# Optimization experiments

Hardware: AMD Instinct MI355X
Metric: run time of the kernel (lower is better)

The kernel has to match this reference:

```python
import jax, jax.numpy as jnp
import numpy as np
from jax import lax

R_NOBOUNDARY, R_BOUNDARY, SMALL_M, BIG_M = 5, 20, 3, 6
NUM_CLASSES, EMBED = 20, 2048


def _conv1d(x, w, pad):
    # x: [B, Cin, T], w: [Cout, Cin, K] -> [B, Cout, T]
    return lax.conv_general_dilated(x, w, (1,), [(pad, pad)],
                                    dimension_numbers=('NCH', 'OIH', 'NCH'))


def _erode(b, k):
    # scipy binary_erosion with structure ones((1,k)), border_value=0:
    # out[i] = min over window [i - k//2, i + k-1 - k//2], zero-padded
    c = k // 2
    xp = jnp.pad(b, ((0, 0), (c, k - 1 - c)))
    return lax.reduce_window(xp, jnp.inf, lax.min, (1, k), (1, 1), 'VALID')


def _dilate(b, k):
    # scipy binary_dilation reflects the structure: window [i-(k-1-c), i+c]
    c = k // 2
    xp = jnp.pad(b, ((0, 0), (k - 1 - c, c)))
    return lax.reduce_window(xp, -jnp.inf, lax.max, (1, k), (1, 1), 'VALID')


def _select_topk(scores, emb, k):
    # scores: [B,T], emb: [B,T,D] -> ([B,k,D], [B,k])
    _, idx = lax.top_k(scores, k)
    sel = jnp.take_along_axis(emb, idx[:, :, None], axis=1)
    return sel, idx


def setup_inputs() -> dict:
    key = jax.random.key(0)
    ks = jax.random.split(key, 6)
    B, T = 16, 750
    x = jax.random.normal(ks[0], (B, T, 2048), dtype=jnp.float32)
    s_embed = 1.0 / np.sqrt(1024 * 3)
    w_rgb = jax.random.normal(ks[1], (EMBED, 1024, 3), dtype=jnp.float32) * s_embed
    b_rgb = jnp.zeros((EMBED,), dtype=jnp.float32)
    w_flow = jax.random.normal(ks[2], (EMBED, 1024, 3), dtype=jnp.float32) * s_embed
    b_flow = jnp.zeros((EMBED,), dtype=jnp.float32)
    w_cls = jax.random.normal(ks[3], (NUM_CLASSES, EMBED, 1), dtype=jnp.float32) / np.sqrt(EMBED)
    return {'x': x, 'w_rgb': w_rgb, 'b_rgb': b_rgb, 'w_flow': w_flow,
            'b_flow': b_flow, 'w_cls': w_cls}


def reference(x, w_rgb, b_rgb, w_flow, b_flow, w_cls):
    # Dropout layers are identity (eval mode).
    T = x.shape[1]
    k_nb = T // R_NOBOUNDARY
    k_b = T // R_BOUNDARY

    rgb = jnp.transpose(x[:, :, 0:1024], (0, 2, 1))    # [B,1024,T]
    flow = jnp.transpose(x[:, :, 1024:2048], (0, 2, 1))
    out = (jax.nn.relu(_conv1d(rgb, w_rgb, 1) + b_rgb[None, :, None])
           + jax.nn.relu(_conv1d(flow, w_flow, 1) + b_flow[None, :, None]))  # [B,2048,T]
    embeddings = jnp.transpose(out, (0, 2, 1))          # [B,T,2048]
    cas = jnp.transpose(jax.nn.relu(_conv1d(out, w_cls, 0)), (0, 2, 1))  # [B,T,C]
    actionness = cas.sum(axis=2)                        # [B,T]

    # no-boundary mining (dropout identity in eval)
    act_rev = jnp.max(actionness, axis=1, keepdims=True) - actionness
    EA, idx = _select_topk(actionness, embeddings, k_nb)
    EB, _ = _select_topk(act_rev, embeddings, k_nb)

    # boundary mining via 1D morphology on binarized actionness
    med = jnp.median(actionness, axis=1, keepdims=True)
    aness_bin = (actionness > med).astype(actionness.dtype)  # [B,T]
    inner = _erode(aness_bin, SMALL_M) - _erode(aness_bin, BIG_M)
    HA, _ = _select_topk(actionness * inner, embeddings, k_b)
    outer = _dilate(aness_bin, BIG_M) - _dilate(aness_bin, SMALL_M)
    HB, _ = _select_topk(actionness * outer, embeddings, k_b)

    # video-level class scores: per-class top-k mean over time, softmax over classes
    cas_ct = jnp.transpose(cas, (0, 2, 1))              # [B,C,T]
    topk_scores, _ = lax.top_k(cas_ct, k_nb)            # [B,C,k_nb]
    video_scores = jax.nn.softmax(topk_scores.mean(axis=2), axis=1)  # [B,C]

    return (video_scores, EA, EB, HA, HB, idx, actionness, cas, embeddings)
```

## Files before the change

### kernel.cpp

```cpp
#include <hip/hip_runtime.h>
#include <stdint.h>
#include <math.h>

#define B_   16
#define T_   750
#define NC_  20
#define KNB_ 150
#define KB_  37

typedef _Float16 f16x8 __attribute__((ext_vector_type(8)));
typedef _Float16 f16x4 __attribute__((ext_vector_type(4)));
typedef float    f32x4 __attribute__((ext_vector_type(4)));
typedef float    f32x16 __attribute__((ext_vector_type(16)));

static constexpr long long O_VS  = 0;
static constexpr long long O_EA  = 320;
static constexpr long long O_EB  = 320 + 4915200LL;
static constexpr long long O_HA  = 320 + 2*4915200LL;
static constexpr long long O_HB  = O_HA + 1212416LL;
static constexpr long long O_IDX = O_HB + 1212416LL;
static constexpr long long O_ACT = O_IDX + 2400LL;
static constexpr long long O_CAS = O_ACT + 12000LL;
static constexpr long long O_EMB = O_CAS + 240000LL;

static constexpr long long WX_ELE   = 16LL * 752 * 2048;
static constexpr long long W_XHI    = 0;
static constexpr long long W_XLO    = W_XHI + WX_ELE * 2;
static constexpr long long WW_ELE   = 2LL * 16 * 32 * 12288;
static constexpr long long W_WHI    = W_XLO + WX_ELE * 2;
static constexpr long long W_WLO    = W_WHI + WW_ELE * 2;
static constexpr long long W_SEL    = W_WLO + WW_ELE * 2;
static constexpr long long W_VS     = W_SEL + 40960;
static constexpr long long W_NEED   = W_VS + 4096;

__device__ __forceinline__ void gload16(const void* g, void* l) {
    __builtin_amdgcn_global_load_lds(
        (const __attribute__((address_space(1))) unsigned int*)g,
        (__attribute__((address_space(3))) unsigned int*)l, 16, 0, 0);
}

__global__ __launch_bounds__(256) void xsplit(
    const float* __restrict__ x, _Float16* __restrict__ xh, _Float16* __restrict__ xl)
{
    long i = (long)blockIdx.x * 256 + threadIdx.x;
    int row = (int)(i >> 9);
    int c4  = (int)(i & 511);
    int b = row / 752, tr = row - b * 752;
    int t = tr - 1;
    float4 v = make_float4(0.f, 0.f, 0.f, 0.f);
    if (t >= 0 && t < T_)
        v = *reinterpret_cast<const float4*>(x + ((long)(b * T_ + t) * 2048 + c4 * 4));
    float vv[4] = {v.x, v.y, v.z, v.w};
    f16x4 h, l;
    #pragma unroll
    for (int j = 0; j < 4; ++j) {
        _Float16 hi = (_Float16)vv[j];
        h[j] = hi;
        l[j] = (_Float16)(vv[j] - (float)hi);
    }
    long o = (long)row * 2048 + c4 * 4;
    *reinterpret_cast<f16x4*>(xh + o) = h;
    *reinterpret_cast<f16x4*>(xl + o) = l;
}

__global__ __launch_bounds__(64) void wsplit(
    const float* __restrict__ w_rgb, const float* __restrict__ w_flow,
    _Float16* __restrict__ wh, _Float16* __restrict__ wl)
{
    const int br   = blockIdx.x >> 11;
    const int co_g = blockIdx.x & 2047;
    const int tid  = threadIdx.x;
    const float* w = (br ? w_flow : w_rgb) + (long)co_g * 3072;
    __shared__ float wsrc[3072];
    for (int i = tid; i < 768; i += 64)
        reinterpret_cast<float4*>(wsrc)[i] = reinterpret_cast<const float4*>(w)[i];
    __syncthreads();
    const int nt = co_g >> 7, co = co_g & 127;
    for (int p = tid; p < 384; p += 64) {
        int oct = p / 3, k = p - oct * 3;
        int chunk = oct >> 2, g = oct & 3;
        int q = g ^ ((co >> 1) & 3);
        f16x8 h, l;
        #pragma unroll
        for (int j = 0; j < 8; ++j) {
            float v = wsrc[(oct * 8 + j) * 3 + k] * 512.f;
            _Float16 hi = (_Float16)v;
            h[j] = hi;
            l[j] = (_Float16)(v - (float)hi);
        }
        long o = ((long)(br * 16 + nt) * 32 + chunk) * 12288 + k * 4096 + co * 32 + q * 8;
        *reinterpret_cast<f16x8*>(wh + o) = h;
        *reinterpret_cast<f16x8*>(wl + o) = l;
    }
}

template<int ADD>
__global__ __launch_bounds__(256, 2) void conv_mfma(
    const _Float16* __restrict__ xh, const _Float16* __restrict__ xl,
    const _Float16* __restrict__ wh, const _Float16* __restrict__ wl,
    const float* __restrict__ bias, float* __restrict__ emb)
{
    __shared__ _Float16 XhL[6272], XlL[6272];
    __shared__ _Float16 WhL[12288], WlL[12288];

    const int tid  = threadIdx.x;
    const int lane = tid & 63;
    const int wid  = tid >> 6;
    const int wm = wid >> 1, wn = wid & 1;
    const int l31 = lane & 31, lg2 = lane >> 5;

    const int bid = blockIdx.y * 16 + blockIdx.x;
    const int lid = (bid & 7) * 128 + (bid >> 3);
    const int nt  = lid >> 6;
    const int bty = lid & 63;
    const int b   = bty >> 2;
    const int tt  = bty & 3;
    const int t0  = tt * 192;

    f32x16 acc[3][2];
    #pragma unroll
    for (int m = 0; m < 3; ++m)
        #pragma unroll
        for (int n = 0; n < 2; ++n)
            #pragma unroll
            for (int e = 0; e < 16; ++e) acc[m][n][e] = 0.f;

    const long xrowbase = (long)b * 752 + t0;
    for (int chunk = 0; chunk < 32; ++chunk) {
        const int cibase = ADD * 1024 + chunk * 32;
        for (int s = tid; s < 776; s += 256) {
            int r = s >> 2, q = s & 3;
            int g = q ^ ((r >> 1) & 3);
            long goff = (xrowbase + r) * 2048 + cibase + g * 8;
            int lbase = (s & ~63) * 8;
            gload16(xh + goff, XhL + lbase);
            gload16(xl + goff, XlL + lbase);
        }
        const long wbase = ((long)(ADD * 16 + nt) * 32 + chunk) * 12288;
        for (int s = tid; s < 1536; s += 256) {
            int lbase = (s & ~63) * 8;
            gload16(wh + wbase + (long)s * 8, WhL + lbase);
            gload16(wl + wbase + (long)s * 8, WlL + lbase);
        }
        __syncthreads();

        #pragma unroll
        for (int k = 0; k < 3; ++k) {
            #pragma unroll
            for (int s2 = 0; s2 < 2; ++s2) {
                const int g = 2 * s2 + lg2;
                f16x8 ah[3], al[3], bh[2], bl[2];
                #pragma unroll
                for (int m = 0; m < 3; ++m) {
                    int r = wm * 96 + m * 32 + l31 + k;
                    int off = r * 32 + ((g ^ ((r >> 1) & 3)) * 8);
                    ah[m] = *reinterpret_cast<const f16x8*>(&XhL[off]);
                    al[m] = *reinterpret_cast<const f16x8*>(&XlL[off]);
                }
                #pragma unroll
                for (int n = 0; n < 2; ++n) {
                    int co = wn * 64 + n * 32 + l31;
                    int off = k * 4096 + co * 32 + ((g ^ ((co >> 1) & 3)) * 8);
                    bh[n] = *reinterpret_cast<const f16x8*>(&WhL[off]);
                    bl[n] = *reinterpret_cast<const f16x8*>(&WlL[off]);
                }
                #pragma unroll
                for (int m = 0; m < 3; ++m)
                    #pragma unroll
                    for (int n = 0; n < 2; ++n) {
                        acc[m][n] = __builtin_amdgcn_mfma_f32_32x32x16_f16(ah[m], bh[n], acc[m][n], 0, 0, 0);
                        acc[m][n] = __builtin_amdgcn_mfma_f32_32x32x16_f16(al[m], bh[n], acc[m][n], 0, 0, 0);
                        acc[m][n] = __builtin_amdgcn_mfma_f32_32x32x16_f16(ah[m], bl[n], acc[m][n], 0, 0, 0);
                    }
            }
        }
        __syncthreads();
    }

    const float sc = 1.f / 512.f;
    #pragma unroll
    for (int n = 0; n < 2; ++n) {
        const int co = nt * 128 + wn * 64 + n * 32 + l31;
        const float bs = bias[co];
        #pragma unroll
        for (int m = 0; m < 3; ++m) {
            #pragma unroll
            for (int reg = 0; reg < 16; ++reg) {
                int row32 = (reg & 3) + 8 * (reg >> 2) + 4 * lg2;
                int t = t0 + wm * 96 + m * 32 + row32;
                if (t < T_) {
                    long o = ((long)b * T_ + t) * 2048 + co;
                    float v = fmaxf(fmaf(acc[m][n][reg], sc, bs), 0.f);
                    if (ADD) emb[o] += v;
                    else     emb[o]  = v;
                }
            }
        }
    }
}

__global__ __launch_bounds__(320) void cas_tc(
    const float* __restrict__ emb, const float* __restrict__ wcls,
    float* __restrict__ cas, float* __restrict__ act)
{
    const int t0g = blockIdx.x * 16;
    const int tid = threadIdx.x;
    const int tl  = tid / 20, c = tid % 20;
    __shared__ float embS[16][132];
    __shared__ float wS[20][132];
    __shared__ float casS[16][20];

    float acc = 0.f;
    for (int cc = 0; cc < 2048; cc += 128) {
        for (int s = tid; s < 512; s += 320) {
            int r = s >> 5, q = s & 31;
            *reinterpret_cast<float4*>(&embS[r][q * 4]) =
                *reinterpret_cast<const float4*>(&emb[((long)t0g + r) * 2048 + cc + q * 4]);
        }
        for (int s = tid; s < 640; s += 320) {
            int r = s >> 5, q = s & 31;
            *reinterpret_cast<float4*>(&wS[r][q * 4]) =
                *reinterpret_cast<const float4*>(&wcls[(long)r * 2048 + cc + q * 4]);
        }
        __syncthreads();
        #pragma unroll
        for (int q = 0; q < 32; ++q) {
            float4 a = *reinterpret_cast<const float4*>(&embS[tl][q * 4]);
            float4 w = *reinterpret_cast<const float4*>(&wS[c][q * 4]);
            acc = fmaf(a.x, w.x, acc); acc = fmaf(a.y, w.y, acc);
            acc = fmaf(a.z, w.z, acc); acc = fmaf(a.w, w.w, acc);
        }
        __syncthreads();
    }
    float r = acc > 0.f ? acc : 0.f;
    cas[(long)(t0g + tl) * NC_ + c] = r;
    casS[tl][c] = r;
    __syncthreads();
    if (tid < 16) {
        float s = 0.f;
        #pragma unroll
        for (int c2 = 0; c2 < NC_; ++c2) s += casS[tid][c2];
        act[t0g + tid] = s;
    }
}

__global__ __launch_bounds__(256) void conv_embed_f32(
    const float* __restrict__ x,
    const float* __restrict__ w_rgb, const float* __restrict__ b_rgb,
    const float* __restrict__ w_flow, const float* __restrict__ b_flow,
    float* __restrict__ emb)
{
    __shared__ float Xs[2][16][132];
    __shared__ float Ws[2][16][3][68];
    const int tid = threadIdx.x;
    const int tx  = tid & 15;
    const int ty  = tid >> 4;
    const int co0 = blockIdx.x * 64;
    const int tb  = blockIdx.y;
    const int t0  = (tb % 6) * 128;
    const int b   = tb / 6;
    const float* xb = x + (long long)b * T_ * 2048;
    float acc[2][8][4];
    #pragma unroll
    for (int br = 0; br < 2; ++br)
        #pragma unroll
        for (int i = 0; i < 8; ++i)
            #pragma unroll
            for (int j = 0; j < 4; ++j) acc[br][i][j] = 0.f;
    for (int cc = 0; cc < 1024; cc += 16) {
        for (int it = tid; it < 1040; it += 256) {
            int br = (it >= 520);
            int r4 = it - br * 520;
            int r  = r4 >> 2;
            int cq = r4 & 3;
            int t  = t0 - 1 + r;
            float4 v = make_float4(0.f, 0.f, 0.f, 0.f);
            if (t >= 0 && t < T_)
                v = *reinterpret_cast<const float4*>(xb + (long long)t * 2048 + br * 1024 + cc + cq * 4);
            Xs[br][cq * 4 + 0][r] = v.x;
            Xs[br][cq * 4 + 1][r] = v.y;
            Xs[br][cq * 4 + 2][r] = v.z;
            Xs[br][cq * 4 + 3][r] = v.w;
        }
        for (int it = tid; it < 1536; it += 256) {
            int br = (it >= 768);
            int r  = it - br * 768;
            int co = r / 12;
            int fq = r - co * 12;
            const float* wsrc = (br ? w_flow : w_rgb) + ((long long)(co0 + co) * 1024 + cc) * 3 + fq * 4;
            float4 v = *reinterpret_cast<const float4*>(wsrc);
            float vv[4] = {v.x, v.y, v.z, v.w};
            #pragma unroll
            for (int j = 0; j < 4; ++j) {
                int f  = fq * 4 + j;
                int ci = f / 3;
                int kk = f - ci * 3;
                Ws[br][ci][kk][co] = vv[j];
            }
        }
        __syncthreads();
        #pragma unroll
        for (int ci = 0; ci < 16; ++ci) {
            float xr[2][12];
            #pragma unroll
            for (int br = 0; br < 2; ++br) {
                const float4* xp = reinterpret_cast<const float4*>(&Xs[br][ci][ty * 8]);
                float4 a0 = xp[0], a1 = xp[1], a2 = xp[2];
                xr[br][0] = a0.x; xr[br][1] = a0.y; xr[br][2]  = a0.z; xr[br][3]  = a0.w;
                xr[br][4] = a1.x; xr[br][5] = a1.y; xr[br][6]  = a1.z; xr[br][7]  = a1.w;
                xr[br][8] = a2.x; xr[br][9] = a2.y; xr[br][10] = a2.z; xr[br][11] = a2.w;
            }
            #pragma unroll
            for (int br = 0; br < 2; ++br) {
                #pragma unroll
                for (int k = 0; k < 3; ++k) {
                    const float4 bv = *reinterpret_cast<const float4*>(&Ws[br][ci][k][tx * 4]);
                    float bw[4] = {bv.x, bv.y, bv.z, bv.w};
                    #pragma unroll
                    for (int i = 0; i < 8; ++i)
                        #pragma unroll
                        for (int j = 0; j < 4; ++j)
                            acc[br][i][j] = fmaf(xr[br][i + k], bw[j], acc[br][i][j]);
                }
            }
        }
        __syncthreads();
    }
    const float4 brv = *reinterpret_cast<const float4*>(b_rgb + co0 + tx * 4);
    const float4 bfv = *reinterpret_cast<const float4*>(b_flow + co0 + tx * 4);
    float brr[4] = {brv.x, brv.y, brv.z, brv.w};
    float bff[4] = {bfv.x, bfv.y, bfv.z, bfv.w};
    #pragma unroll
    for (int i = 0; i < 8; ++i) {
        int t = t0 + ty * 8 + i;
        if (t < T_) {
            float ov[4];
            #pragma unroll
            for (int j = 0; j < 4; ++j) {
                float r = acc[0][i][j] + brr[j];
                float f = acc[1][i][j] + bff[j];
                r = r > 0.f ? r : 0.f;
                f = f > 0.f ? f : 0.f;
                ov[j] = r + f;
            }
            float4 o; o.x = ov[0]; o.y = ov[1]; o.z = ov[2]; o.w = ov[3];
            *reinterpret_cast<float4*>(emb + ((long long)b * T_ + t) * 2048 + co0 + tx * 4) = o;
        }
    }
}

__device__ inline float keyval(unsigned long long k) {
    return __uint_as_float(~(unsigned)(k >> 32));
}

__device__ inline void bitonic_sort_u64(unsigned long long* keys, int tid)
{
    for (unsigned size = 2; size <= 1024; size <<= 1) {
        for (unsigned stride = size >> 1; stride > 0; stride >>= 1) {
            __syncthreads();
            for (int j = tid; j < 512; j += 256) {
                unsigned i = ((j & ~(stride - 1)) << 1) | (j & (stride - 1));
                unsigned p = i + stride;
                bool asc = ((i & size) == 0);
                unsigned long long a = keys[i];
                unsigned long long c = keys[p];
                bool sw = asc ? (a > c) : (a < c);
                if (sw) { keys[i] = c; keys[p] = a; }
            }
        }
    }
    __syncthreads();
}

__device__ inline void bitonic_sort_u32(unsigned* keys, int tid)
{
    for (unsigned size = 2; size <= 1024; size <<= 1) {
        for (unsigned stride = size >> 1; stride > 0; stride >>= 1) {
            __syncthreads();
            for (int j = tid; j < 512; j += 256) {
                unsigned i = ((j & ~(stride - 1)) << 1) | (j & (stride - 1));
                unsigned p = i + stride;
                bool asc = ((i & size) == 0);
                unsigned a = keys[i];
                unsigned c = keys[p];
                bool sw = asc ? (a > c) : (a < c);
                if (sw) { keys[i] = c; keys[p] = a; }
            }
        }
    }
    __syncthreads();
}

__global__ __launch_bounds__(256) void analysis_kernel(
    const float* __restrict__ act, float* __restrict__ idx_out, int* __restrict__ sel)
{
    const int b   = blockIdx.x;
    const int tid = threadIdx.x;
    __shared__ float av[T_];
    __shared__ unsigned long long keys[1024];
    __shared__ unsigned char bin[T_];
    __shared__ float medmax[2];

    for (int t = tid; t < T_; t += 256) av[t] = act[b * T_ + t];
    __syncthreads();

    for (int p = tid; p < 1024; p += 256) {
        unsigned long long k = ~0ull;
        if (p < T_) k = ((unsigned long long)(~__float_as_uint(av[p])) << 32) | (unsigned)p;
        keys[p] = k;
    }
    bitonic_sort_u64(keys, tid);
    if (tid < KNB_) {
        int t = (int)(keys[tid] & 0xffffffffu);
        idx_out[b * KNB_ + tid] = (float)t;
        sel[(b * 4 + 0) * 160 + tid] = t;
    }
    if (tid == 0) {
        medmax[0] = 0.5f * (keyval(keys[374]) + keyval(keys[375]));
        medmax[1] = keyval(keys[0]);
    }
    __syncthreads();
    const float med = medmax[0];
    const float mx  = medmax[1];
    for (int t = tid; t < T_; t += 256) bin[t] = (av[t] > med) ? 1 : 0;
    __syncthreads();

    for (int p = tid; p < 1024; p += 256) {
        unsigned long long k = ~0ull;
        if (p < T_) k = ((unsigned long long)(~__float_as_uint(mx - av[p])) << 32) | (unsigned)p;
        keys[p] = k;
    }
    bitonic_sort_u64(keys, tid);
    if (tid < KNB_) sel[(b * 4 + 1) * 160 + tid] = (int)(keys[tid] & 0xffffffffu);
    __syncthreads();

    for (int p = tid; p < 1024; p += 256) {
        unsigned long long k = ~0ull;
        if (p < T_) {
            int b0 = (p >= 1) ? bin[p - 1] : 0;
            int b1 = bin[p];
            int b2 = (p + 1 < T_) ? bin[p + 1] : 0;
            int e3 = b0 & b1 & b2;
            int e6 = 1;
            #pragma unroll
            for (int d = -3; d <= 2; ++d) {
                int q = p + d;
                e6 &= (q >= 0 && q < T_) ? (int)bin[q] : 0;
            }
            float s = (e3 && !e6) ? av[p] : 0.f;
            k = ((unsigned long long)(~__float_as_uint(s)) << 32) | (unsigned)p;
        }
        keys[p] = k;
    }
    bitonic_sort_u64(keys, tid);
    if (tid < KB_) sel[(b * 4 + 2) * 160 + tid] = (int)(keys[tid] & 0xffffffffu);
    __syncthreads();

    for (int p = tid; p < 1024; p += 256) {
        unsigned long long k = ~0ull;
        if (p < T_) {
            int b0 = (p >= 1) ? bin[p - 1] : 0;
            int b1 = bin[p];
            int b2 = (p + 1 < T_) ? bin[p + 1] : 0;
            int d3 = b0 | b1 | b2;
            int d6 = 0;
            #pragma unroll
            for (int d = -2; d <= 3; ++d) {
                int q = p + d;
                d6 |= (q >= 0 && q < T_) ? (int)bin[q] : 0;
            }
            float s = (d6 && !d3) ? av[p] : 0.f;
            k = ((unsigned long long)(~__float_as_uint(s)) << 32) | (unsigned)p;
        }
        keys[p] = k;
    }
    bitonic_sort_u64(keys, tid);
    if (tid < KB_) sel[(b * 4 + 3) * 160 + tid] = (int)(keys[tid] & 0xffffffffu);
}

__global__ __launch_bounds__(256) void video_topk(
    const float* __restrict__ cas, float* __restrict__ vs)
{
    const int bc  = blockIdx.x;
    const int b   = bc / NC_;
    const int c   = bc - b * NC_;
    const int tid = threadIdx.x;
    __shared__ unsigned keys[1024];
    __shared__ float red[4];
    for (int p = tid; p < 1024; p += 256)
        keys[p] = (p < T_) ? ~__float_as_uint(cas[((long long)b * T_ + p) * NC_ + c]) : 0xffffffffu;
    bitonic_sort_u32(keys, tid);
    float v = (tid < KNB_) ? __uint_as_float(~keys[tid]) : 0.f;
    #pragma unroll
    for (int off = 32; off > 0; off >>= 1) v += __shfl_down(v, off, 64);
    const int lane = tid & 63, wid = tid >> 6;
    if (lane == 0) red[wid] = v;
    __syncthreads();
    if (tid == 0) vs[bc] = (red[0] + red[1] + red[2] + red[3]) / 150.f;
}

__global__ void softmax20(const float* __restrict__ vs, float* __restrict__ out)
{
    const int b   = blockIdx.x;
    const int tid = threadIdx.x;
    float v = (tid < NC_) ? vs[b * NC_ + tid] : -INFINITY;
    float m = v;
    #pragma unroll
    for (int off = 32; off > 0; off >>= 1) m = fmaxf(m, __shfl_xor(m, off, 64));
    float e = (tid < NC_) ? expf(v - m) : 0.f;
    float s = e;
    #pragma unroll
    for (int off = 32; off > 0; off >>= 1) s += __shfl_xor(s, off, 64);
    if (tid < NC_) out[b * NC_ + tid] = e / s;
}

__global__ __launch_bounds__(256) void gather_rows(
    const float* __restrict__ emb, const int* __restrict__ sel, float* __restrict__ out)
{
    const int r = blockIdx.x;
    const int b = r / 374;
    const int q = r - b * 374;
    int g, p; long long dst;
    if (q < 150)      { g = 0; p = q;       dst = O_EA + (long long)(b * KNB_ + p) * 2048; }
    else if (q < 300) { g = 1; p = q - 150; dst = O_EB + (long long)(b * KNB_ + p) * 2048; }
    else if (q < 337) { g = 2; p = q - 300; dst = O_HA + (long long)(b * KB_ + p) * 2048; }
    else              { g = 3; p = q - 337; dst = O_HB + (long long)(b * KB_ + p) * 2048; }
    const int t = sel[(b * 4 + g) * 160 + p];
    const float4* src = reinterpret_cast<const float4*>(emb + ((long long)b * T_ + t) * 2048);
    float4* d = reinterpret_cast<float4*>(out + dst);
    for (int i = threadIdx.x; i < 512; i += 256) d[i] = src[i];
}

extern "C" void kernel_launch(void* const* d_in, const int* in_sizes, int n_in,
                              void* d_out, int out_size, void* d_ws, size_t ws_size,
                              hipStream_t stream)
{
    const float* x      = (const float*)d_in[0];
    const float* w_rgb  = (const float*)d_in[1];
    const float* b_rgb  = (const float*)d_in[2];
    const float* w_flow = (const float*)d_in[3];
    const float* b_flow = (const float*)d_in[4];
    const float* w_cls  = (const float*)d_in[5];

    float* out  = (float*)d_out;
    float* emb  = out + O_EMB;
    float* cas  = out + O_CAS;
    float* act  = out + O_ACT;
    float* idxo = out + O_IDX;

    const bool fast = (ws_size >= (size_t)W_NEED);

    int*   sel;
    float* vs;
    if (fast) {
        sel = (int*)((char*)d_ws + W_SEL);
        vs  = (float*)((char*)d_ws + W_VS);
        _Float16* xh = (_Float16*)((char*)d_ws + W_XHI);
        _Float16* xl = (_Float16*)((char*)d_ws + W_XLO);
        _Float16* wh = (_Float16*)((char*)d_ws + W_WHI);
        _Float16* wl = (_Float16*)((char*)d_ws + W_WLO);

        xsplit<<<24064, 256, 0, stream>>>(x, xh, xl);
        wsplit<<<4096, 64, 0, stream>>>(w_rgb, w_flow, wh, wl);
        conv_mfma<0><<<dim3(16, 64), 256, 0, stream>>>(xh, xl, wh, wl, b_rgb, emb);
        conv_mfma<1><<<dim3(16, 64), 256, 0, stream>>>(xh, xl, wh, wl, b_flow, emb);
    } else {
        sel = (int*)d_ws;
        vs  = (float*)((char*)d_ws + 64 * 1024);
        conv_embed_f32<<<dim3(32, 96), 256, 0, stream>>>(x, w_rgb, b_rgb, w_flow, b_flow, emb);
    }

    cas_tc<<<750, 320, 0, stream>>>(emb, w_cls, cas, act);
    analysis_kernel<<<B_, 256, 0, stream>>>(act, idxo, sel);
    video_topk<<<B_ * NC_, 256, 0, stream>>>(cas, vs);
    softmax20<<<B_, 64, 0, stream>>>(vs, out + O_VS);
    gather_rows<<<B_ * 374, 256, 0, stream>>>(emb, sel, out);
}
```

Baseline: 1.254 ms.

## Hold conv weights in registers with 16x16 MFMA; split analysis into parallel top-k blocks

The conv kernel stops staging weights through shared memory. Each wave now loads its weight fragments straight from global memory into registers (unswizzled layout) and switches from 32x32x16 to 16x16x32 MFMA tiles with a 6x4 accumulator grid. Block indexing is also simplified, dropping the XCD-aware remap. Separately, the single-block-per-batch analysis kernel becomes a median/max kernel plus a 64-block top-k kernel that runs the four sorts in parallel with 512-thread bitonic passes. These changes cut LDS traffic and the serial sort latency, at the risk of global-load latency inside the MFMA loop and higher register pressure.

Measured after the change: 1.137 ms. -9.4%, faster.

```diff
diff --git a/kernel.cpp b/kernel.cpp
--- a/kernel.cpp
+++ b/kernel.cpp
@@ -11,7 +11,6 @@
 typedef _Float16 f16x8 __attribute__((ext_vector_type(8)));
 typedef _Float16 f16x4 __attribute__((ext_vector_type(4)));
 typedef float    f32x4 __attribute__((ext_vector_type(4)));
-typedef float    f32x16 __attribute__((ext_vector_type(16)));
 
 static constexpr long long O_VS  = 0;
 static constexpr long long O_EA  = 320;
@@ -31,7 +30,8 @@
 static constexpr long long W_WLO    = W_WHI + WW_ELE * 2;
 static constexpr long long W_SEL    = W_WLO + WW_ELE * 2;
 static constexpr long long W_VS     = W_SEL + 40960;
-static constexpr long long W_NEED   = W_VS + 4096;
+static constexpr long long W_MED    = W_VS + 4096;
+static constexpr long long W_NEED   = W_MED + 256;
 
 __device__ __forceinline__ void gload16(const void* g, void* l) {
     __builtin_amdgcn_global_load_lds(
@@ -79,7 +79,6 @@
     for (int p = tid; p < 384; p += 64) {
         int oct = p / 3, k = p - oct * 3;
         int chunk = oct >> 2, g = oct & 3;
-        int q = g ^ ((co >> 1) & 3);
         f16x8 h, l;
         #pragma unroll
         for (int j = 0; j < 8; ++j) {
@@ -88,7 +87,7 @@
             h[j] = hi;
             l[j] = (_Float16)(v - (float)hi);
         }
-        long o = ((long)(br * 16 + nt) * 32 + chunk) * 12288 + k * 4096 + co * 32 + q * 8;
+        long o = ((long)(br * 16 + nt) * 32 + chunk) * 12288 + k * 4096 + co * 32 + g * 8;
         *reinterpret_cast<f16x8*>(wh + o) = h;
         *reinterpret_cast<f16x8*>(wl + o) = l;
     }
@@ -101,33 +100,38 @@
     const float* __restrict__ bias, float* __restrict__ emb)
 {
     __shared__ _Float16 XhL[6272], XlL[6272];
-    __shared__ _Float16 WhL[12288], WlL[12288];
 
     const int tid  = threadIdx.x;
     const int lane = tid & 63;
     const int wid  = tid >> 6;
     const int wm = wid >> 1, wn = wid & 1;
-    const int l31 = lane & 31, lg2 = lane >> 5;
-
-    const int bid = blockIdx.y * 16 + blockIdx.x;
-    const int lid = (bid & 7) * 128 + (bid >> 3);
-    const int nt  = lid >> 6;
-    const int bty = lid & 63;
-    const int b   = bty >> 2;
-    const int tt  = bty & 3;
-    const int t0  = tt * 192;
-
-    f32x16 acc[3][2];
-    #pragma unroll
-    for (int m = 0; m < 3; ++m)
-        #pragma unroll
-        for (int n = 0; n < 2; ++n)
-            #pragma unroll
-            for (int e = 0; e < 16; ++e) acc[m][n][e] = 0.f;
+    const int lrow = lane & 15, lg = lane >> 4;
+    const int nt = blockIdx.x;
+    const int b  = blockIdx.y >> 2;
+    const int tt = blockIdx.y & 3;
+    const int t0 = tt * 192;
+
+    f32x4 acc[6][4];
+    #pragma unroll
+    for (int m = 0; m < 6; ++m)
+        #pragma unroll
+        for (int n = 0; n < 4; ++n)
+            acc[m][n] = (f32x4){0.f, 0.f, 0.f, 0.f};
 
     const long xrowbase = (long)b * 752 + t0;
+    const int  cibase0  = ADD * 1024;
+    const long wslice   = ((long)(ADD * 16 + nt) * 32) * 12288;
+    const int  wlane    = (wn * 64 + lrow) * 32 + lg * 8;
+
     for (int chunk = 0; chunk < 32; ++chunk) {
-        const int cibase = ADD * 1024 + chunk * 32;
+        const long wb = wslice + (long)chunk * 12288 + wlane;
+        f16x8 bh0[4], bl0[4], bh1[4], bl1[4];
+        #pragma unroll
+        for (int n = 0; n < 4; ++n) {
+            bh0[n] = *reinterpret_cast<const f16x8*>(wh + wb + n * 512);
+            bl0[n] = *reinterpret_cast<const f16x8*>(wl + wb + n * 512);
+        }
+        const int cibase = cibase0 + chunk * 32;
         for (int s = tid; s < 776; s += 256) {
             int r = s >> 2, q = s & 3;
             int g = q ^ ((r >> 1) & 3);
@@ -136,42 +140,55 @@
             gload16(xh + goff, XhL + lbase);
             gload16(xl + goff, XlL + lbase);
         }
-        const long wbase = ((long)(ADD * 16 + nt) * 32 + chunk) * 12288;
-        for (int s = tid; s < 1536; s += 256) {
-            int lbase = (s & ~63) * 8;
-            gload16(wh + wbase + (long)s * 8, WhL + lbase);
-            gload16(wl + wbase + (long)s * 8, WlL + lbase);
-        }
         __syncthreads();
 
         #pragma unroll
-        for (int k = 0; k < 3; ++k) {
-            #pragma unroll
-            for (int s2 = 0; s2 < 2; ++s2) {
-                const int g = 2 * s2 + lg2;
-                f16x8 ah[3], al[3], bh[2], bl[2];
-                #pragma unroll
-                for (int m = 0; m < 3; ++m) {
-                    int r = wm * 96 + m * 32 + l31 + k;
-                    int off = r * 32 + ((g ^ ((r >> 1) & 3)) * 8);
-                    ah[m] = *reinterpret_cast<const f16x8*>(&XhL[off]);
-                    al[m] = *reinterpret_cast<const f16x8*>(&XlL[off]);
-                }
-                #pragma unroll
-                for (int n = 0; n < 2; ++n) {
-                    int co = wn * 64 + n * 32 + l31;
-                    int off = k * 4096 + co * 32 + ((g ^ ((co >> 1) & 3)) * 8);
-                    bh[n] = *reinterpret_cast<const f16x8*>(&WhL[off]);
-                    bl[n] = *reinterpret_cast<const f16x8*>(&WlL[off]);
-                }
-                #pragma unroll
-                for (int m = 0; m < 3; ++m)
-                    #pragma unroll
-                    for (int n = 0; n < 2; ++n) {
-                        acc[m][n] = __builtin_amdgcn_mfma_f32_32x32x16_f16(ah[m], bh[n], acc[m][n], 0, 0, 0);
-                        acc[m][n] = __builtin_amdgcn_mfma_f32_32x32x16_f16(al[m], bh[n], acc[m][n], 0, 0, 0);
-                        acc[m][n] = __builtin_amdgcn_mfma_f32_32x32x16_f16(ah[m], bl[n], acc[m][n], 0, 0, 0);
-                    }
+        for (int n = 0; n < 4; ++n) {
+            bh1[n] = *reinterpret_cast<const f16x8*>(wh + wb + 4096 + n * 512);
+            bl1[n] = *reinterpret_cast<const f16x8*>(wl + wb + 4096 + n * 512);
+        }
+        #pragma unroll
+        for (int m = 0; m < 6; ++m) {
+            int r = wm * 96 + m * 16 + lrow;
+            int off = r * 32 + ((lg ^ ((r >> 1) & 3)) * 8);
+            f16x8 ah = *reinterpret_cast<const f16x8*>(&XhL[off]);
+            f16x8 al = *reinterpret_cast<const f16x8*>(&XlL[off]);
+            #pragma unroll
+            for (int n = 0; n < 4; ++n) {
+                acc[m][n] = __builtin_amdgcn_mfma_f32_16x16x32_f16(ah, bh0[n], acc[m][n], 0, 0, 0);
+                acc[m][n] = __builtin_amdgcn_mfma_f32_16x16x32_f16(al, bh0[n], acc[m][n], 0, 0, 0);
+                acc[m][n] = __builtin_amdgcn_mfma_f32_16x16x32_f16(ah, bl0[n], acc[m][n], 0, 0, 0);
+            }
+        }
+        #pragma unroll
+        for (int n = 0; n < 4; ++n) {
+            bh0[n] = *reinterpret_cast<const f16x8*>(wh + wb + 8192 + n * 512);
+            bl0[n] = *reinterpret_cast<const f16x8*>(wl + wb + 8192 + n * 512);
+        }
+        #pragma unroll
+        for (int m = 0; m < 6; ++m) {
+            int r = wm * 96 + m * 16 + lrow + 1;
+            int off = r * 32 + ((lg ^ ((r >> 1) & 3)) * 8);
+            f16x8 ah = *reinterpret_cast<const f16x8*>(&XhL[off]);
+            f16x8 al = *reinterpret_cast<const f16x8*>(&XlL[off]);
+            #pragma unroll
+            for (int n = 0; n < 4; ++n) {
+                acc[m][n] = __builtin_amdgcn_mfma_f32_16x16x32_f16(ah, bh1[n], acc[m][n], 0, 0, 0);
+                acc[m][n] = __builtin_amdgcn_mfma_f32_16x16x32_f16(al, bh1[n], acc[m][n], 0, 0, 0);
+                acc[m][n] = __builtin_amdgcn_mfma_f32_16x16x32_f16(ah, bl1[n], acc[m][n], 0, 0, 0);
+            }
+        }
+        #pragma unroll
+        for (int m = 0; m < 6; ++m) {
+            int r = wm * 96 + m * 16 + lrow + 2;
+            int off = r * 32 + ((lg ^ ((r >> 1) & 3)) * 8);
+            f16x8 ah = *reinterpret_cast<const f16x8*>(&XhL[off]);
+            f16x8 al = *reinterpret_cast<const f16x8*>(&XlL[off]);
+            #pragma unroll
+            for (int n = 0; n < 4; ++n) {
+                acc[m][n] = __builtin_amdgcn_mfma_f32_16x16x32_f16(ah, bh0[n], acc[m][n], 0, 0, 0);
+                acc[m][n] = __builtin_amdgcn_mfma_f32_16x16x32_f16(al, bh0[n], acc[m][n], 0, 0, 0);
+                acc[m][n] = __builtin_amdgcn_mfma_f32_16x16x32_f16(ah, bl0[n], acc[m][n], 0, 0, 0);
             }
         }
         __syncthreads();
@@ -179,18 +196,17 @@
 
     const float sc = 1.f / 512.f;
     #pragma unroll
-    for (int n = 0; n < 2; ++n) {
-        const int co = nt * 128 + wn * 64 + n * 32 + l31;
+    for (int n = 0; n < 4; ++n) {
+        const int co = nt * 128 + wn * 64 + n * 16 + lrow;
         const float bs = bias[co];
         #pragma unroll
-        for (int m = 0; m < 3; ++m) {
-            #pragma unroll
-            for (int reg = 0; reg < 16; ++reg) {
-                int row32 = (reg & 3) + 8 * (reg >> 2) + 4 * lg2;
-                int t = t0 + wm * 96 + m * 32 + row32;
+        for (int m = 0; m < 6; ++m) {
+            #pragma unroll
+            for (int rg = 0; rg < 4; ++rg) {
+                int t = t0 + wm * 96 + m * 16 + lg * 4 + rg;
                 if (t < T_) {
                     long o = ((long)b * T_ + t) * 2048 + co;
-                    float v = fmaxf(fmaf(acc[m][n][reg], sc, bs), 0.f);
+                    float v = fmaxf(fmaf(acc[m][n][rg], sc, bs), 0.f);
                     if (ADD) emb[o] += v;
                     else     emb[o]  = v;
                 }
@@ -349,30 +365,45 @@
     }
 }
 
-__device__ inline float keyval(unsigned long long k) {
+__device__ inline float keyval64(unsigned long long k) {
     return __uint_as_float(~(unsigned)(k >> 32));
 }
 
-__device__ inline void bitonic_sort_u64(unsigned long long* keys, int tid)
+__device__ inline void bitonic512_u64(unsigned long long* keys, int tid)
 {
     for (unsigned size = 2; size <= 1024; size <<= 1) {
         for (unsigned stride = size >> 1; stride > 0; stride >>= 1) {
             __syncthreads();
-            for (int j = tid; j < 512; j += 256) {
-                unsigned i = ((j & ~(stride - 1)) << 1) | (j & (stride - 1));
-                unsigned p = i + stride;
-                bool asc = ((i & size) == 0);
-                unsigned long long a = keys[i];
-                unsigned long long c = keys[p];
-                bool sw = asc ? (a > c) : (a < c);
-                if (sw) { keys[i] = c; keys[p] = a; }
-            }
-        }
-    }
-    __syncthreads();
-}
-
-__device__ inline void bitonic_sort_u32(unsigned* keys, int tid)
+            unsigned i = ((tid & ~(stride - 1)) << 1) | (tid & (stride - 1));
+            unsigned p = i + stride;
+            bool asc = ((i & size) == 0);
+            unsigned long long a = keys[i];
+            unsigned long long c = keys[p];
+            bool sw = asc ? (a > c) : (a < c);
+            if (sw) { keys[i] = c; keys[p] = a; }
+        }
+    }
+    __syncthreads();
+}
+
+__device__ inline void bitonic512_u32(unsigned* keys, int tid)
+{
+    for (unsigned size = 2; size <= 1024; size <<= 1) {
+        for (unsigned stride = size >> 1; stride > 0; stride >>= 1) {
+            __syncthreads();
+            unsigned i = ((tid & ~(stride - 1)) << 1) | (tid & (stride - 1));
+            unsigned p = i + stride;
+            bool asc = ((i & size) == 0);
+            unsigned a = keys[i];
+            unsigned c = keys[p];
+            bool sw = asc ? (a > c) : (a < c);
+            if (sw) { keys[i] = c; keys[p] = a; }
+        }
+    }
+    __syncthreads();
+}
+
+__device__ inline void bitonic_sort_u32_256(unsigned* keys, int tid)
 {
     for (unsigned size = 2; size <= 1024; size <<= 1) {
         for (unsigned stride = size >> 1; stride > 0; stride >>= 1) {
@@ -391,91 +422,85 @@
     __syncthreads();
 }
 
-__global__ __launch_bounds__(256) void analysis_kernel(
-    const float* __restrict__ act, float* __restrict__ idx_out, int* __restrict__ sel)
+__global__ __launch_bounds__(512) void median_max(
+    const float* __restrict__ act, float* __restrict__ medmax)
 {
     const int b   = blockIdx.x;
     const int tid = threadIdx.x;
+    __shared__ unsigned keys[1024];
+    for (int p = tid; p < 1024; p += 512)
+        keys[p] = (p < T_) ? ~__float_as_uint(act[b * T_ + p]) : 0xffffffffu;
+    bitonic512_u32(keys, tid);
+    if (tid == 0) {
+        float v374 = __uint_as_float(~keys[374]);
+        float v375 = __uint_as_float(~keys[375]);
+        medmax[b * 2 + 0] = 0.5f * (v374 + v375);
+        medmax[b * 2 + 1] = __uint_as_float(~keys[0]);
+    }
+}
+
+__global__ __launch_bounds__(512) void topk4(
+    const float* __restrict__ act, const float* __restrict__ medmax,
+    float* __restrict__ idx_out, int* __restrict__ sel)
+{
+    const int b     = blockIdx.x >> 2;
+    const int which = blockIdx.x & 3;
+    const int tid   = threadIdx.x;
     __shared__ float av[T_];
+    __shared__ unsigned char bin[T_];
     __shared__ unsigned long long keys[1024];
-    __shared__ unsigned char bin[T_];
-    __shared__ float medmax[2];
-
-    for (int t = tid; t < T_; t += 256) av[t] = act[b * T_ + t];
-    __syncthreads();
-
-    for (int p = tid; p < 1024; p += 256) {
-        unsigned long long k = ~0ull;
-        if (p < T_) k = ((unsigned long long)(~__float_as_uint(av[p])) << 32) | (unsigned)p;
-        keys[p] = k;
-    }
-    bitonic_sort_u64(keys, tid);
-    if (tid < KNB_) {
-        int t = (int)(keys[tid] & 0xffffffffu);
-        idx_out[b * KNB_ + tid] = (float)t;
-        sel[(b * 4 + 0) * 160 + tid] = t;
-    }
-    if (tid == 0) {
-        medmax[0] = 0.5f * (keyval(keys[374]) + keyval(keys[375]));
-        medmax[1] = keyval(keys[0]);
-    }
-    __syncthreads();
-    const float med = medmax[0];
-    const float mx  = medmax[1];
-    for (int t = tid; t < T_; t += 256) bin[t] = (av[t] > med) ? 1 : 0;
-    __syncthreads();
-
-    for (int p = tid; p < 1024; p += 256) {
-        unsigned long long k = ~0ull;
-        if (p < T_) k = ((unsigned long long)(~__float_as_uint(mx - av[p])) << 32) | (unsigned)p;
-        keys[p] = k;
-    }
-    bitonic_sort_u64(keys, tid);
-    if (tid < KNB_) sel[(b * 4 + 1) * 160 + tid] = (int)(keys[tid] & 0xffffffffu);
-    __syncthreads();
-
-    for (int p = tid; p < 1024; p += 256) {
+
+    for (int t = tid; t < T_; t += 512) av[t] = act[b * T_ + t];
+    const float med = medmax[b * 2 + 0];
+    const float mx  = medmax[b * 2 + 1];
+    __syncthreads();
+    if (which >= 2)
+        for (int t = tid; t < T_; t += 512) bin[t] = (av[t] > med) ? 1 : 0;
+    __syncthreads();
+
+    for (int p = tid; p < 1024; p += 512) {
         unsigned long long k = ~0ull;
         if (p < T_) {
-            int b0 = (p >= 1) ? bin[p - 1] : 0;
-            int b1 = bin[p];
-            int b2 = (p + 1 < T_) ? bin[p + 1] : 0;
-            int e3 = b0 & b1 & b2;
-            int e6 = 1;
-            #pragma unroll
-            for (int d = -3; d <= 2; ++d) {
-                int q = p + d;
-                e6 &= (q >= 0 && q < T_) ? (int)bin[q] : 0;
-            }
-            float s = (e3 && !e6) ? av[p] : 0.f;
+            float s;
+            if (which == 0) s = av[p];
+            else if (which == 1) s = mx - av[p];
+            else if (which == 2) {
+                int b0 = (p >= 1) ? bin[p - 1] : 0;
+                int b1 = bin[p];
+                int b2 = (p + 1 < T_) ? bin[p + 1] : 0;
+                int e3 = b0 & b1 & b2;
+                int e6 = 1;
+                #pragma unroll
+                for (int d = -3; d <= 2; ++d) {
+                    int q = p + d;
+                    e6 &= (q >= 0 && q < T_) ? (int)bin[q] : 0;
+                }
+                s = (e3 && !e6) ? av[p] : 0.f;
+            } else {
+                int b0 = (p >= 1) ? bin[p - 1] : 0;
+                int b1 = bin[p];
+                int b2 = (p + 1 < T_) ? bin[p + 1] : 0;
+                int d3 = b0 | b1 | b2;
+                int d6 = 0;
+                #pragma unroll
+                for (int d = -2; d <= 3; ++d) {
+                    int q = p + d;
+                    d6 |= (q >= 0 && q < T_) ? (int)bin[q] : 0;
+                }
+                s = (d6 && !d3) ? av[p] : 0.f;
+            }
             k = ((unsigned long long)(~__float_as_uint(s)) << 32) | (unsigned)p;
         }
         keys[p] = k;
     }
-    bitonic_sort_u64(keys, tid);
-    if (tid < KB_) sel[(b * 4 + 2) * 160 + tid] = (int)(keys[tid] & 0xffffffffu);
-    __syncthreads();
-
-    for (int p = tid; p < 1024; p += 256) {
-        unsigned long long k = ~0ull;
-        if (p < T_) {
-            int b0 = (p >= 1) ? bin[p - 1] : 0;
-            int b1 = bin[p];
-            int b2 = (p + 1 < T_) ? bin[p + 1] : 0;
-            int d3 = b0 | b1 | b2;
-            int d6 = 0;
-            #pragma unroll
-            for (int d = -2; d <= 3; ++d) {
-                int q = p + d;
-                d6 |= (q >= 0 && q < T_) ? (int)bin[q] : 0;
-            }
-            float s = (d6 && !d3) ? av[p] : 0.f;
-            k = ((unsigned long long)(~__float_as_uint(s)) << 32) | (unsigned)p;
-        }
-        keys[p] = k;
-    }
-    bitonic_sort_u64(keys, tid);
-    if (tid < KB_) sel[(b * 4 + 3) * 160 + tid] = (int)(keys[tid] & 0xffffffffu);
+    bitonic512_u64(keys, tid);
+
+    const int kn = (which < 2) ? KNB_ : KB_;
+    if (tid < kn) {
+        int t = (int)(keys[tid] & 0xffffffffu);
+        sel[(b * 4 + which) * 160 + tid] = t;
+        if (which == 0) idx_out[b * KNB_ + tid] = (float)t;
+    }
 }
 
 __global__ __launch_bounds__(256) void video_topk(
@@ -489,7 +514,7 @@
     __shared__ float red[4];
     for (int p = tid; p < 1024; p += 256)
         keys[p] = (p < T_) ? ~__float_as_uint(cas[((long long)b * T_ + p) * NC_ + c]) : 0xffffffffu;
-    bitonic_sort_u32(keys, tid);
+    bitonic_sort_u32_256(keys, tid);
     float v = (tid < KNB_) ? __uint_as_float(~keys[tid]) : 0.f;
     #pragma unroll
     for (int off = 32; off > 0; off >>= 1) v += __shfl_down(v, off, 64);
@@ -552,9 +577,11 @@
 
     int*   sel;
     float* vs;
+    float* medmax;
     if (fast) {
-        sel = (int*)((char*)d_ws + W_SEL);
-        vs  = (float*)((char*)d_ws + W_VS);
+        sel    = (int*)((char*)d_ws + W_SEL);
+        vs     = (float*)((char*)d_ws + W_VS);
+        medmax = (float*)((char*)d_ws + W_MED);
         _Float16* xh = (_Float16*)((char*)d_ws + W_XHI);
         _Float16* xl = (_Float16*)((char*)d_ws + W_XLO);
         _Float16* wh = (_Float16*)((char*)d_ws + W_WHI);
@@ -565,13 +592,15 @@
         conv_mfma<0><<<dim3(16, 64), 256, 0, stream>>>(xh, xl, wh, wl, b_rgb, emb);
         conv_mfma<1><<<dim3(16, 64), 256, 0, stream>>>(xh, xl, wh, wl, b_flow, emb);
     } else {
-        sel = (int*)d_ws;
-        vs  = (float*)((char*)d_ws + 64 * 1024);
+        sel    = (int*)d_ws;
+        vs     = (float*)((char*)d_ws + 40960);
+        medmax = (float*)((char*)d_ws + 40960 + 4096);
         conv_embed_f32<<<dim3(32, 96), 256, 0, stream>>>(x, w_rgb, b_rgb, w_flow, b_flow, emb);
     }
 
     cas_tc<<<750, 320, 0, stream>>>(emb, w_cls, cas, act);
-    analysis_kernel<<<B_, 256, 0, stream>>>(act, idxo, sel);
+    median_max<<<B_, 512, 0, stream>>>(act, medmax);
+    topk4<<<B_ * 4, 512, 0, stream>>>(act, medmax, idxo, sel);
     video_topk<<<B_ * NC_, 256, 0, stream>>>(cas, vs);
     softmax20<<<B_, 64, 0, stream>>>(vs, out + O_VS);
     gather_rows<<<B_ * 374, 256, 0, stream>>>(emb, sel, out);
```
